# Kernel tuning notes

Measured on AMD Instinct MI355X. Metric: run time of the kernel, lower is better.

Reference implementation:

```python
import jax, jax.numpy as jnp
import numpy as np

MAX_FREQ = 3
OMEGA = 0.5 * np.pi
SQRT2 = float(np.sqrt(2.0))


def _embed(x, max_freq, omega):
    # x: (Q,) -> (Q, 2*max_freq+1) : [1, sqrt2*cos(1*w*x), sqrt2*sin(1*w*x), ...]
    freqs = jnp.arange(1, max_freq + 1, dtype=x.dtype) * jnp.asarray(omega, x.dtype)
    ang = x[:, None] * freqs  # (Q, n)
    cs = jnp.stack([jnp.cos(ang), jnp.sin(ang)], axis=-1).reshape(x.shape[0], 2 * max_freq)
    return jnp.concatenate([jnp.ones((x.shape[0], 1), x.dtype), SQRT2 * cs], axis=-1)


def setup_inputs() -> dict:
    key = jax.random.key(0)
    feat = jax.random.normal(key, (4, 147, 64, 64), dtype=jnp.float32)
    return {"feat": feat, "h": 256, "w": 256, "flip1": 1, "flip3": 2}


def reference(feat, h, w, flip1, flip3):
    N, C3, H, W = feat.shape
    c = C3 // 3  # (2*max_freq+1)^2
    n1 = 2 * MAX_FREQ + 1
    dt = feat.dtype
    Q = h * w

    # make_coord((h, w)): centers of grid cells in [-1, 1]; channel0 over h-axis
    xs = (-1.0 + (2.0 * jnp.arange(h, dtype=dt) + 1.0) / h)
    ys = (-1.0 + (2.0 * jnp.arange(w, dtype=dt) + 1.0) / w)
    cx, cy = jnp.meshgrid(xs, ys, indexing='ij')
    coord = jnp.stack([cx.ravel(), cy.ravel()], axis=-1)  # (Q, 2)
    if flip1 == 1:
        coord = coord * jnp.array([1.0, -1.0], dtype=dt)
    elif flip1 == 2:
        coord = coord * jnp.array([-1.0, 1.0], dtype=dt)
    elif flip1 == 4:
        coord = -coord

    rx = 1.0 / H  # 2 / H / 2
    ry = 1.0 / W
    eps_shift = 1e-06

    feat_flat = jnp.transpose(feat, (0, 2, 3, 1)).reshape(N, H * W, C3)  # (N, H*W, C3)

    preds = []
    areas = []
    for vx in (-1, 1):
        for vy in (-1, 1):
            shift = jnp.array([vx * rx + eps_shift, vy * ry + eps_shift], dtype=dt)
            coord_ = jnp.clip(coord + shift, -1.0 + 1e-06, 1.0 - 1e-06)  # (Q, 2)
            # grid_sample nearest, align_corners=False: unnormalize then round-half-even
            ih = jnp.clip(jnp.round(((coord_[:, 0] + 1.0) * H - 1.0) * 0.5).astype(jnp.int32), 0, H - 1)
            iw = jnp.clip(jnp.round(((coord_[:, 1] + 1.0) * W - 1.0) * 0.5).astype(jnp.int32), 0, W - 1)
            latent = jnp.take(feat_flat, ih * W + iw, axis=1)  # (N, Q, 3c)
            # q_coord equals cell-center coords at the gathered index
            qh = -1.0 + (2.0 * ih.astype(dt) + 1.0) / H
            qw = -1.0 + (2.0 * iw.astype(dt) + 1.0) / W
            rel0 = (coord[:, 0] - qh) * H  # (Q,)
            rel1 = (coord[:, 1] - qw) * W
            if flip3 == 1:
                rel1 = -rel1
            elif flip3 == 2:
                rel0 = -rel0
            elif flip3 == 4:
                rel0, rel1 = -rel0, -rel1
            ex = _embed(rel0, MAX_FREQ, OMEGA)  # (Q, n1)
            ey = _embed(rel1, MAX_FREQ, OMEGA)
            ope = (ex[:, :, None] * ey[:, None, :]).reshape(Q, c)  # (Q, c)
            pred = jnp.einsum('qc,nqkc->nqk', ope, latent.reshape(N, Q, 3, c))  # (N, Q, 3)
            preds.append(pred)
            areas.append(jnp.abs(rel0 * rel1) + 1e-09)

    tot_area = areas[0] + areas[1] + areas[2] + areas[3]  # (Q,)
    areas = [areas[3], areas[2], areas[1], areas[0]]  # diagonal swap
    ret = preds[0] * (areas[0] / tot_area)[None, :, None]
    for p, a in zip(preds[1:], areas[1:]):
        ret = ret + p * (a / tot_area)[None, :, None]
    return jnp.transpose(ret.reshape(N, h, w, 3), (0, 3, 1, 2))
```

## Files before the change

kernel.cpp:

```cpp
#include <hip/hip_runtime.h>
#include <math.h>


#define FH 64
#define FW 64
#define NC3 147
#define OHW 256
#define CPAD 52
#define LDSZ (2 * FW * CPAD)

__device__ __forceinline__ void embed7(float r, float e[7]) {
    const float F1  = 1.5707963705062866f;
    const float SQ2 = 1.4142135381698608f;
    float a = r * F1;
    float s1 = __sinf(a), c1 = __cosf(a);
    float s2 = 2.0f * s1 * c1, c2 = c1 * c1 - s1 * s1;
    float s3 = s2 * c1 + c2 * s1, c3 = c2 * c1 - s2 * s1;
    e[0] = 1.0f;
    e[1] = SQ2 * c1; e[2] = SQ2 * s1;
    e[3] = SQ2 * c2; e[4] = SQ2 * s2;
    e[5] = SQ2 * c3; e[6] = SQ2 * s3;
}

__global__ __launch_bounds__(256, 3) void ope_render_kernel(
    const float* __restrict__ feat,
    const int* __restrict__ pflip1,
    const int* __restrict__ pflip3,
    float* __restrict__ out)
{
    __shared__ float lds[LDSZ];

    const int tid = threadIdx.x;
    const int k   = blockIdx.x;
    const int ib  = blockIdx.y;
    const int n   = blockIdx.z;
    const int flip1 = pflip1[0];
    const int flip3 = pflip3[0];

    const int rA = (ib == 0) ? 0  : (ib - 1);
    const int rB = (ib == 0) ? 63 : ib;

    float4 sv[7];
    {
        const int cbase = k * 49;
        #pragma unroll
        for (int it = 0; it < 7; ++it) {
            int u = tid + it * 256;
            if (u < 2 * 13 * FW) {
                int col = u & 63;
                int d   = (u >> 6) & 1;
                int g   = u >> 7;
                int row = d ? rB : rA;
                const float* __restrict__ src =
                    feat + (((size_t)n * NC3 + cbase + 4 * g) * FH + row) * FW + col;
                float4 v;
                v.x = src[0];
                v.y = (4 * g + 1 < 49) ? src[FH * FW]     : 0.0f;
                v.z = (4 * g + 2 < 49) ? src[2 * FH * FW] : 0.0f;
                v.w = (4 * g + 3 < 49) ? src[3 * FH * FW] : 0.0f;
                sv[it] = v;
            }
        }
    }

    const int m  = tid >> 6;
    const int jg = tid & 63;
    const bool fx = (flip1 == 2) || (flip1 == 4);
    const bool fy = (flip1 == 1) || (flip1 == 4);
    const bool o  = (jg == 0);

    const float SHm = (float)(-1.0 / 64.0 + 1e-6);
    const float SHp = (float)( 1.0 / 64.0 + 1e-6);
    const float CLO = (float)(-1.0 + 1e-6);
    const float CHI = (float)( 1.0 - 1e-6);

    const int i_e = (ib == 0) ? ((m < 2) ? m : 252 + m) : (4 * ib - 2 + m);
    const float cx = -1.0f + (2.0f * (float)i_e + 1.0f) * (1.0f / 256.0f);

    float rel0[2]; int rl[2];
    #pragma unroll
    for (int dx = 0; dx < 2; ++dx) {
        float sh = dx ? SHp : SHm;
        float c0 = fminf(fmaxf(cx + sh, CLO), CHI);
        int ih = (int)rintf(((c0 + 1.0f) * 64.0f - 1.0f) * 0.5f);
        ih = min(max(ih, 0), FH - 1);
        rl[dx] = (ih == rB) ? 1 : 0;
        float qh = -1.0f + (2.0f * (float)ih + 1.0f) * (1.0f / 64.0f);
        rel0[dx] = (cx - qh) * 64.0f;
    }

    float r0a = rel0[0], r0b = rel0[1];
    if (flip3 == 2 || flip3 == 4) { r0a = -r0a; r0b = -r0b; }
    float ex[2][7];
    embed7(r0a, ex[0]); embed7(r0b, ex[1]);

    {
        #pragma unroll
        for (int it = 0; it < 7; ++it) {
            int u = tid + it * 256;
            if (u < 2 * 13 * FW) {
                int col = u & 63;
                int d   = (u >> 6) & 1;
                int g   = u >> 7;
                *(float4*)&lds[(size_t)((d << 6) + col) * CPAD + 4 * g] = sv[it];
            }
        }
    }
    __syncthreads();

    float tp[2][7];
    #pragma unroll
    for (int dx = 0; dx < 2; ++dx) {
        const float4* __restrict__ vp =
            (const float4*)&lds[(size_t)((rl[dx] << 6) + jg) * CPAD];
        float mreg[52];
        #pragma unroll
        for (int g = 0; g < 13; ++g) {
            float4 t = vp[g];
            mreg[4*g] = t.x; mreg[4*g+1] = t.y; mreg[4*g+2] = t.z; mreg[4*g+3] = t.w;
        }
        #pragma unroll
        for (int b = 0; b < 7; ++b) {
            float s = ex[dx][0] * mreg[b];
            #pragma unroll
            for (int a = 1; a < 7; ++a) s = fmaf(ex[dx][a], mreg[7*a + b], s);
            tp[dx][b] = s;
        }
    }

    const int srcl = (jg + 63) & 63;
    float qv[2][7];
    #pragma unroll
    for (int dx = 0; dx < 2; ++dx)
        #pragma unroll
        for (int b = 0; b < 7; ++b)
            qv[dx][b] = __shfl(tp[dx][b], srcl, 64);

    const int colU1 = o ? 63 : jg;
    float acc0, acc1, acc2, acc3;
    #pragma unroll
    for (int p = 0; p < 2; ++p) {
        const int jb = o ? (p ? 254 : 0) : (4 * jg - 2 + 2 * p);
        const float cyp = -1.0f + (2.0f * (float)jb + 1.0f) * (1.0f / 256.0f);
        float qw[2]; bool cs[2];
        #pragma unroll
        for (int dy = 0; dy < 2; ++dy) {
            float sh = dy ? SHp : SHm;
            float c1 = fminf(fmaxf(cyp + sh, CLO), CHI);
            int iw = (int)rintf(((c1 + 1.0f) * 64.0f - 1.0f) * 0.5f);
            iw = min(max(iw, 0), FW - 1);
            cs[dy] = (iw == colU1);
            qw[dy] = -1.0f + (2.0f * (float)iw + 1.0f) * (1.0f / 64.0f);
        }
        float cvs[2][2][7];
        #pragma unroll
        for (int dy = 0; dy < 2; ++dy) {
            const bool selP = cs[dy] != o;
            #pragma unroll
            for (int dx = 0; dx < 2; ++dx)
                #pragma unroll
                for (int b = 0; b < 7; ++b)
                    cvs[dy][dx][b] = selP ? tp[dx][b] : qv[dx][b];
        }
        #pragma unroll
        for (int sub = 0; sub < 2; ++sub) {
            const int j_e = jb + sub;
            const float cy = -1.0f + (2.0f * (float)j_e + 1.0f) * (1.0f / 256.0f);
            float rel1_0 = (cy - qw[0]) * 64.0f;
            float rel1_1 = (cy - qw[1]) * 64.0f;

            float a00 = fabsf(rel0[0] * rel1_0) + 1e-9f;
            float a01 = fabsf(rel0[0] * rel1_1) + 1e-9f;
            float a10 = fabsf(rel0[1] * rel1_0) + 1e-9f;
            float a11 = fabsf(rel0[1] * rel1_1) + 1e-9f;
            float tot = ((a00 + a01) + a10) + a11;
            float rinv = 1.0f / tot;
            float w00 = a11 * rinv, w01 = a10 * rinv, w10 = a01 * rinv, w11 = a00 * rinv;

            float r1a = rel1_0, r1b = rel1_1;
            if (flip3 == 1 || flip3 == 4) { r1a = -r1a; r1b = -r1b; }
            float ey0[7], ey1[7];
            embed7(r1a, ey0); embed7(r1b, ey1);

            float v00 = 0.0f, v01 = 0.0f, v10 = 0.0f, v11 = 0.0f;
            #pragma unroll
            for (int b = 0; b < 7; ++b) {
                v00 = fmaf(cvs[0][0][b], ey0[b], v00);
                v10 = fmaf(cvs[0][1][b], ey0[b], v10);
                v01 = fmaf(cvs[1][0][b], ey1[b], v01);
                v11 = fmaf(cvs[1][1][b], ey1[b], v11);
            }
            float r = fmaf(v00, w00, fmaf(v01, w01, fmaf(v10, w10, v11 * w11)));
            if (p == 0) { if (sub == 0) acc0 = r; else acc1 = r; }
            else        { if (sub == 0) acc2 = r; else acc3 = r; }
        }
    }

    const int i_out = fx ? (255 - i_e) : i_e;
    float* __restrict__ ob = out + (((size_t)n * 3 + k) * OHW + i_out) * OHW;
    const int jA = o ? 0   : (4 * jg - 2);
    const int jB = o ? 254 : (4 * jg);
    if (!fy) {
        *(float2*)&ob[jA] = make_float2(acc0, acc1);
        *(float2*)&ob[jB] = make_float2(acc2, acc3);
    } else {
        *(float2*)&ob[254 - jA] = make_float2(acc1, acc0);
        *(float2*)&ob[254 - jB] = make_float2(acc3, acc2);
    }
}

extern "C" void kernel_launch(void* const* d_in, const int* in_sizes, int n_in,
                              void* d_out, int out_size, void* d_ws, size_t ws_size,
                              hipStream_t stream) {
    const float* feat  = (const float*)d_in[0];
    const int*   flip1 = (const int*)d_in[3];
    const int*   flip3 = (const int*)d_in[4];
    float*       out   = (float*)d_out;

    dim3 grid(3, 64, 4);
    dim3 block(256);
    hipLaunchKernelGGL(ope_render_kernel, grid, block, 0, stream,
                       feat, flip1, flip3, out);
}
```

Measured before the change: 11.93 us.

## Derive neighbor indices analytically and reuse embeddings via parity symmetry

Replaces the per-corner clip/round index computation with closed-form row/column selection, and derives the second x/y embedding from the first by sign flips, since the relative offsets differ by exactly 2 (odd harmonics flip sign, even ones stay). Boundary blocks skip the second LDS row contraction and copy the first. Embedding and area weights are precomputed before the barrier so they can overlap the global loads, and the division becomes a hardware reciprocal. This removes transcendental and ALU work but relies on exact grid geometry assumptions and uses an approximate reciprocal.

```diff
diff --git a/kernel.cpp b/kernel.cpp
--- a/kernel.cpp
+++ b/kernel.cpp
@@ -37,8 +37,9 @@
     const int flip1 = pflip1[0];
     const int flip3 = pflip3[0];
 
-    const int rA = (ib == 0) ? 0  : (ib - 1);
-    const int rB = (ib == 0) ? 63 : ib;
+    const bool boundary = (ib == 0);
+    const int rA = boundary ? 0  : (ib - 1);
+    const int rB = boundary ? 63 : ib;
 
     float4 sv[7];
     {
@@ -68,31 +69,58 @@
     const bool fx = (flip1 == 2) || (flip1 == 4);
     const bool fy = (flip1 == 1) || (flip1 == 4);
     const bool o  = (jg == 0);
-
-    const float SHm = (float)(-1.0 / 64.0 + 1e-6);
-    const float SHp = (float)( 1.0 / 64.0 + 1e-6);
-    const float CLO = (float)(-1.0 + 1e-6);
-    const float CHI = (float)( 1.0 - 1e-6);
-
-    const int i_e = (ib == 0) ? ((m < 2) ? m : 252 + m) : (4 * ib - 2 + m);
+    const float sgx = (flip3 == 2 || flip3 == 4) ? -1.0f : 1.0f;
+    const float sgy = (flip3 == 1 || flip3 == 4) ? -1.0f : 1.0f;
+
+    const int i_e = boundary ? ((m < 2) ? m : 252 + m) : (4 * ib - 2 + m);
     const float cx = -1.0f + (2.0f * (float)i_e + 1.0f) * (1.0f / 256.0f);
-
-    float rel0[2]; int rl[2];
-    #pragma unroll
-    for (int dx = 0; dx < 2; ++dx) {
-        float sh = dx ? SHp : SHm;
-        float c0 = fminf(fmaxf(cx + sh, CLO), CHI);
-        int ih = (int)rintf(((c0 + 1.0f) * 64.0f - 1.0f) * 0.5f);
-        ih = min(max(ih, 0), FH - 1);
-        rl[dx] = (ih == rB) ? 1 : 0;
-        float qh = -1.0f + (2.0f * (float)ih + 1.0f) * (1.0f / 64.0f);
-        rel0[dx] = (cx - qh) * 64.0f;
-    }
-
-    float r0a = rel0[0], r0b = rel0[1];
-    if (flip3 == 2 || flip3 == 4) { r0a = -r0a; r0b = -r0b; }
-    float ex[2][7];
-    embed7(r0a, ex[0]); embed7(r0b, ex[1]);
+    const int d0 = boundary ? (m >> 1) : 0;
+    const int d1 = boundary ? d0       : 1;
+    const int row0 = d0 ? rB : rA;
+    const float qh0 = -1.0f + (2.0f * (float)row0 + 1.0f) * (1.0f / 64.0f);
+    const float rel0_0 = (cx - qh0) * 64.0f;
+    const float rel0_1 = boundary ? rel0_0 : (rel0_0 - 2.0f);
+
+    float ex0[7], ex1[7];
+    embed7(sgx * rel0_0, ex0);
+    {
+        const float xm = boundary ? 1.0f : -1.0f;
+        ex1[0] = 1.0f;
+        ex1[1] = xm * ex0[1]; ex1[2] = xm * ex0[2];
+        ex1[3] = ex0[3];      ex1[4] = ex0[4];
+        ex1[5] = xm * ex0[5]; ex1[6] = xm * ex0[6];
+    }
+
+    const float tm = o ? 0.0f : -2.0f;
+    const float ym = o ? 1.0f : -1.0f;
+    float eyv[2][2][7];
+    float wts[2][2][4];
+    #pragma unroll
+    for (int p = 0; p < 2; ++p) {
+        const int jb = o ? (p ? 254 : 0) : (4 * jg - 2 + 2 * p);
+        const int cm = o ? (p ? 63 : 0) : (jg - 1);
+        const float qwm = -1.0f + (2.0f * (float)cm + 1.0f) * (1.0f / 64.0f);
+        #pragma unroll
+        for (int sub = 0; sub < 2; ++sub) {
+            const int j_e = jb + sub;
+            const float cy = -1.0f + (2.0f * (float)j_e + 1.0f) * (1.0f / 256.0f);
+            const float rel1m = (cy - qwm) * 64.0f;
+            const float rel1p = rel1m + tm;
+
+            float a00 = fabsf(rel0_0 * rel1m) + 1e-9f;
+            float a01 = fabsf(rel0_0 * rel1p) + 1e-9f;
+            float a10 = fabsf(rel0_1 * rel1m) + 1e-9f;
+            float a11 = fabsf(rel0_1 * rel1p) + 1e-9f;
+            float tot = ((a00 + a01) + a10) + a11;
+            float rinv = __builtin_amdgcn_rcpf(tot);
+            wts[p][sub][0] = a11 * rinv;
+            wts[p][sub][1] = a10 * rinv;
+            wts[p][sub][2] = a01 * rinv;
+            wts[p][sub][3] = a00 * rinv;
+
+            embed7(sgy * rel1m, eyv[p][sub]);
+        }
+    }
 
     {
         #pragma unroll
@@ -108,89 +136,86 @@
     }
     __syncthreads();
 
-    float tp[2][7];
-    #pragma unroll
-    for (int dx = 0; dx < 2; ++dx) {
-        const float4* __restrict__ vp =
-            (const float4*)&lds[(size_t)((rl[dx] << 6) + jg) * CPAD];
-        float mreg[52];
+    float cv0[7], cv1[7];
+    #pragma unroll
+    for (int b = 0; b < 7; ++b) { cv0[b] = 0.0f; cv1[b] = 0.0f; }
+    {
+        const float4* __restrict__ bp0 =
+            (const float4*)&lds[(size_t)((d0 << 6) + jg) * CPAD];
         #pragma unroll
         for (int g = 0; g < 13; ++g) {
-            float4 t = vp[g];
-            mreg[4*g] = t.x; mreg[4*g+1] = t.y; mreg[4*g+2] = t.z; mreg[4*g+3] = t.w;
-        }
+            float4 v = bp0[g];
+            float ve[4] = { v.x, v.y, v.z, v.w };
+            #pragma unroll
+            for (int e = 0; e < 4; ++e) {
+                int ch = 4 * g + e;
+                if (ch < 49) cv0[ch % 7] = fmaf(ex0[ch / 7], ve[e], cv0[ch % 7]);
+            }
+        }
+        if (!boundary) {
+            const float4* __restrict__ bp1 =
+                (const float4*)&lds[(size_t)((d1 << 6) + jg) * CPAD];
+            #pragma unroll
+            for (int g = 0; g < 13; ++g) {
+                float4 v = bp1[g];
+                float ve[4] = { v.x, v.y, v.z, v.w };
+                #pragma unroll
+                for (int e = 0; e < 4; ++e) {
+                    int ch = 4 * g + e;
+                    if (ch < 49) cv1[ch % 7] = fmaf(ex1[ch / 7], ve[e], cv1[ch % 7]);
+                }
+            }
+        } else {
+            #pragma unroll
+            for (int b = 0; b < 7; ++b) cv1[b] = cv0[b];
+        }
+    }
+
+    const int srcl = (jg + 63) & 63;
+    float qv0[7], qv1[7];
+    #pragma unroll
+    for (int b = 0; b < 7; ++b) {
+        qv0[b] = __shfl(cv0[b], srcl, 64);
+        qv1[b] = __shfl(cv1[b], srcl, 64);
+    }
+
+    float acc0, acc1, acc2, acc3;
+    #pragma unroll
+    for (int p = 0; p < 2; ++p) {
+        float A0[7], A1[7], B0[7], B1[7];
         #pragma unroll
         for (int b = 0; b < 7; ++b) {
-            float s = ex[dx][0] * mreg[b];
-            #pragma unroll
-            for (int a = 1; a < 7; ++a) s = fmaf(ex[dx][a], mreg[7*a + b], s);
-            tp[dx][b] = s;
-        }
-    }
-
-    const int srcl = (jg + 63) & 63;
-    float qv[2][7];
-    #pragma unroll
-    for (int dx = 0; dx < 2; ++dx)
-        #pragma unroll
-        for (int b = 0; b < 7; ++b)
-            qv[dx][b] = __shfl(tp[dx][b], srcl, 64);
-
-    const int colU1 = o ? 63 : jg;
-    float acc0, acc1, acc2, acc3;
-    #pragma unroll
-    for (int p = 0; p < 2; ++p) {
-        const int jb = o ? (p ? 254 : 0) : (4 * jg - 2 + 2 * p);
-        const float cyp = -1.0f + (2.0f * (float)jb + 1.0f) * (1.0f / 256.0f);
-        float qw[2]; bool cs[2];
-        #pragma unroll
-        for (int dy = 0; dy < 2; ++dy) {
-            float sh = dy ? SHp : SHm;
-            float c1 = fminf(fmaxf(cyp + sh, CLO), CHI);
-            int iw = (int)rintf(((c1 + 1.0f) * 64.0f - 1.0f) * 0.5f);
-            iw = min(max(iw, 0), FW - 1);
-            cs[dy] = (iw == colU1);
-            qw[dy] = -1.0f + (2.0f * (float)iw + 1.0f) * (1.0f / 64.0f);
-        }
-        float cvs[2][2][7];
-        #pragma unroll
-        for (int dy = 0; dy < 2; ++dy) {
-            const bool selP = cs[dy] != o;
-            #pragma unroll
-            for (int dx = 0; dx < 2; ++dx)
-                #pragma unroll
-                for (int b = 0; b < 7; ++b)
-                    cvs[dy][dx][b] = selP ? tp[dx][b] : qv[dx][b];
+            if (p == 0) {
+                A0[b] = o ? cv0[b] : qv0[b];
+                A1[b] = o ? cv1[b] : qv1[b];
+                B0[b] = cv0[b];
+                B1[b] = cv1[b];
+            } else {
+                A0[b] = qv0[b];
+                A1[b] = qv1[b];
+                B0[b] = o ? qv0[b] : cv0[b];
+                B1[b] = o ? qv1[b] : cv1[b];
+            }
         }
         #pragma unroll
         for (int sub = 0; sub < 2; ++sub) {
-            const int j_e = jb + sub;
-            const float cy = -1.0f + (2.0f * (float)j_e + 1.0f) * (1.0f / 256.0f);
-            float rel1_0 = (cy - qw[0]) * 64.0f;
-            float rel1_1 = (cy - qw[1]) * 64.0f;
-
-            float a00 = fabsf(rel0[0] * rel1_0) + 1e-9f;
-            float a01 = fabsf(rel0[0] * rel1_1) + 1e-9f;
-            float a10 = fabsf(rel0[1] * rel1_0) + 1e-9f;
-            float a11 = fabsf(rel0[1] * rel1_1) + 1e-9f;
-            float tot = ((a00 + a01) + a10) + a11;
-            float rinv = 1.0f / tot;
-            float w00 = a11 * rinv, w01 = a10 * rinv, w10 = a01 * rinv, w11 = a00 * rinv;
-
-            float r1a = rel1_0, r1b = rel1_1;
-            if (flip3 == 1 || flip3 == 4) { r1a = -r1a; r1b = -r1b; }
-            float ey0[7], ey1[7];
-            embed7(r1a, ey0); embed7(r1b, ey1);
+            const float* ey0 = eyv[p][sub];
+            float ey1[7];
+            ey1[0] = 1.0f;
+            ey1[1] = ym * ey0[1]; ey1[2] = ym * ey0[2];
+            ey1[3] = ey0[3];      ey1[4] = ey0[4];
+            ey1[5] = ym * ey0[5]; ey1[6] = ym * ey0[6];
 
             float v00 = 0.0f, v01 = 0.0f, v10 = 0.0f, v11 = 0.0f;
             #pragma unroll
             for (int b = 0; b < 7; ++b) {
-                v00 = fmaf(cvs[0][0][b], ey0[b], v00);
-                v10 = fmaf(cvs[0][1][b], ey0[b], v10);
-                v01 = fmaf(cvs[1][0][b], ey1[b], v01);
-                v11 = fmaf(cvs[1][1][b], ey1[b], v11);
-            }
-            float r = fmaf(v00, w00, fmaf(v01, w01, fmaf(v10, w10, v11 * w11)));
+                v00 = fmaf(A0[b], ey0[b], v00);
+                v10 = fmaf(A1[b], ey0[b], v10);
+                v01 = fmaf(B0[b], ey1[b], v01);
+                v11 = fmaf(B1[b], ey1[b], v11);
+            }
+            const float* w = wts[p][sub];
+            float r = fmaf(v00, w[0], fmaf(v01, w[1], fmaf(v10, w[2], v11 * w[3])));
             if (p == 0) { if (sub == 0) acc0 = r; else acc1 = r; }
             else        { if (sub == 0) acc2 = r; else acc3 = r; }
         }
```

Measured after the change: 13.06 us. 9.4% more time.
